# Optimization experiments

Hardware: AMD Instinct MI355X
Metric: run time of the kernel (lower is better)

Reference implementation:

```python
import jax, jax.numpy as jnp
import numpy as np

STRIDES = (4, 8, 16, 32, 64, 128)
MAPS = (128, 64, 32, 16, 8, 4)
VAR0, VAR1 = 0.1, 0.2
CLS_TH, NMS_TH, FINAL_TH = 0.05, 0.3, 0.5


def _decode_scale(ocls, oreg, stride):
    # ocls: [1,2,H,W], oreg: [1,4,H,W] -> dets [H*W, 5] = (x1,y1,x2,y2,score)
    prob = jax.nn.softmax(ocls, axis=1)[0, 1]          # [H,W] face probability
    H, W = prob.shape
    s = jnp.float32(stride)
    pcx = s / 2 + jnp.arange(W, dtype=jnp.float32)[None, :] * s   # prior center x
    pcy = s / 2 + jnp.arange(H, dtype=jnp.float32)[:, None] * s   # prior center y
    pwh = s * 4.0                                                 # prior w = h = 4*stride
    loc = oreg[0]                                                 # [4,H,W]
    cx = pcx + loc[0] * VAR0 * pwh
    cy = pcy + loc[1] * VAR0 * pwh
    w = pwh * jnp.exp(loc[2] * VAR1)
    h = pwh * jnp.exp(loc[3] * VAR1)
    x1 = cx - w / 2
    y1 = cy - h / 2
    x2 = x1 + w
    y2 = y1 + h
    return jnp.stack([x1.ravel(), y1.ravel(), x2.ravel(), y2.ravel(), prob.ravel()], axis=1)


def _nms_keep(dets, valid):
    # Greedy NMS (torch-style, +1 box convention), fixed trip count, returns keep mask.
    N = dets.shape[0]
    scores = jnp.where(valid, dets[:, 4], -jnp.inf)
    order = jnp.argsort(-scores)            # descending by score, invalid last
    b = dets[order]
    v = valid[order]
    x1, y1, x2, y2 = b[:, 0], b[:, 1], b[:, 2], b[:, 3]
    areas = (x2 - x1 + 1.0) * (y2 - y1 + 1.0)
    pos = jnp.arange(N)

    def body(i, carry):
        sup, keep = carry
        active = jnp.logical_and(jnp.logical_not(sup[i]), v[i])
        keep = keep.at[i].set(active)
        xx1 = jnp.maximum(x1[i], x1)
        yy1 = jnp.maximum(y1[i], y1)
        xx2 = jnp.minimum(x2[i], x2)
        yy2 = jnp.minimum(y2[i], y2)
        w = jnp.maximum(xx2 - xx1 + 1.0, 0.0)
        h = jnp.maximum(yy2 - yy1 + 1.0, 0.0)
        inter = w * h
        iou = inter / (areas[i] + areas - inter)
        sup = sup | (active & (iou > NMS_TH) & (pos > i))
        return sup, keep

    sup0 = jnp.logical_not(v)
    _, keep_sorted = jax.lax.fori_loop(0, N, body, (sup0, jnp.zeros(N, dtype=bool)))
    return jnp.zeros(N, dtype=bool).at[order].set(keep_sorted)


def _forward(ol1, ol2, ol3, ol4, ol5, ol6, ol7, ol8, ol9, ol10, ol11, ol12):
    olist = [ol1, ol2, ol3, ol4, ol5, ol6, ol7, ol8, ol9, ol10, ol11, ol12]
    dets = jnp.concatenate(
        [_decode_scale(olist[2 * i], olist[2 * i + 1], STRIDES[i]) for i in range(6)],
        axis=0)                              # [N,5]
    valid = dets[:, 4] > CLS_TH              # threshold stage (score > 0.05)
    # NMS selection is index logic -> constant w.r.t. differentiation
    keep = _nms_keep(jax.lax.stop_gradient(dets), valid)
    final = keep & (dets[:, 4] > FINAL_TH)   # post-NMS score > 0.5 filter
    # fixed-shape equivalent of gathering kept rows: zero out non-kept rows
    return dets * final[:, None].astype(dets.dtype)


def setup_inputs() -> dict:
    key = jax.random.key(0)
    inp = {}
    for i, hw in enumerate(MAPS):
        kc, kr, key = jax.random.split(key, 3)
        inp[f"ol{2 * i + 1}"] = jax.random.normal(kc, (1, 2, hw, hw), dtype=jnp.float32)
        inp[f"ol{2 * i + 2}"] = jax.random.normal(kr, (1, 4, hw, hw), dtype=jnp.float32)
    return inp


def reference(ol1, ol2, ol3, ol4, ol5, ol6, ol7, ol8, ol9, ol10, ol11, ol12):
    return _forward(ol1, ol2, ol3, ol4, ol5, ol6, ol7, ol8, ol9, ol10, ol11, ol12)
```

## Files before the change

### kernel.cpp

```cpp
#include <hip/hip_runtime.h>
#include <stdint.h>

#define N_TOTAL 21840
#define NA      21888
#define W_MAX   342
#define TOT_ENT 3753792u
#define NMS_TH  0.3f
#define FINAL_TH 0.5f
#define NSLICE  8
#define SCAN_T  768
#define NPUSH   11
#define GRP     4
#define NBAND   7
#define GMAX    86

struct Inputs { const float* cls[6]; const float* reg[6]; };

__device__ __forceinline__ void block_bar() {
  asm volatile("s_waitcnt lgkmcnt(0)\n\ts_barrier" ::: "memory");
}

__device__ __forceinline__ unsigned wbase_u(unsigned w) {
  return 64u * (342u * w - (w * (w - 1u)) / 2u);
}

__global__ void decode_kernel(Inputs in,
                              float* __restrict__ dx1, float* __restrict__ dy1,
                              float* __restrict__ dx2, float* __restrict__ dy2,
                              float* __restrict__ dsc,
                              unsigned long long* __restrict__ ckey,
                              unsigned int* __restrict__ Mc,
                              unsigned int* __restrict__ rank32,
                              unsigned int* __restrict__ wcnt,
                              float* __restrict__ out) {
#pragma clang fp contract(off)
  int gid = blockIdx.x * blockDim.x + threadIdx.x;
  if (gid >= N_TOTAL) return;

  rank32[gid] = 0u;
  wcnt[gid] = 0u;
  if (gid < NA - N_TOTAL) wcnt[N_TOTAL + gid] = 0u;

  int sc, local;
  if      (gid < 16384) { sc = 0; local = gid;         }
  else if (gid < 20480) { sc = 1; local = gid - 16384; }
  else if (gid < 21504) { sc = 2; local = gid - 20480; }
  else if (gid < 21760) { sc = 3; local = gid - 21504; }
  else if (gid < 21824) { sc = 4; local = gid - 21760; }
  else                  { sc = 5; local = gid - 21824; }

  const int Wd     = 128 >> sc;
  const int stride = 4 << sc;
  const int HW     = Wd * Wd;
  const int x = local & (Wd - 1);
  const int y = local >> (7 - sc);

  const float* cls = in.cls[sc];
  const float* reg = in.reg[sc];

  float c0 = cls[local];
  float c1 = cls[HW + local];
  float m  = fmaxf(c0, c1);
  float e0 = expf(c0 - m);
  float e1 = expf(c1 - m);
  float prob = e1 / (e0 + e1);

  float l0 = reg[local];
  float l1 = reg[HW + local];
  float l2 = reg[2 * HW + local];
  float l3 = reg[3 * HW + local];

  float sF  = (float)stride;
  float pcx = 0.5f * sF + (float)x * sF;
  float pcy = 0.5f * sF + (float)y * sF;
  float pwh = sF * 4.0f;

  float cx = pcx + ((l0 * 0.1f) * pwh);
  float cy = pcy + ((l1 * 0.1f) * pwh);
  float w  = pwh * expf(l2 * 0.2f);
  float h  = pwh * expf(l3 * 0.2f);
  float x1 = cx - w * 0.5f;
  float y1 = cy - h * 0.5f;
  float x2 = x1 + w;
  float y2 = y1 + h;

  dx1[gid] = x1; dy1[gid] = y1; dx2[gid] = x2; dy2[gid] = y2; dsc[gid] = prob;

  out[gid * 5 + 0] = 0.0f;
  out[gid * 5 + 1] = 0.0f;
  out[gid * 5 + 2] = 0.0f;
  out[gid * 5 + 3] = 0.0f;
  out[gid * 5 + 4] = 0.0f;

  if (prob > FINAL_TH) {
    unsigned int pos = atomicAdd(Mc, 1u);
    ckey[pos] = ((unsigned long long)__float_as_uint(prob) << 32) |
                (unsigned int)(~(unsigned int)gid);
  }
}

__global__ void __launch_bounds__(256)
rank_kernel(const unsigned long long* __restrict__ ckey,
            const unsigned int* __restrict__ Mc,
            const float* __restrict__ dx1, const float* __restrict__ dy1,
            const float* __restrict__ dx2, const float* __restrict__ dy2,
            float* __restrict__ sx1, float* __restrict__ sy1,
            float* __restrict__ sx2, float* __restrict__ sy2,
            unsigned int* __restrict__ sorig,
            unsigned int* __restrict__ rank32) {
  __shared__ unsigned long long tile[256];
  const unsigned int M = *Mc;
  if (blockIdx.x * 256u >= M) return;
  const int t = (int)threadIdx.x;
  const int p = (int)blockIdx.x * 256 + t;
  unsigned long long mykey = (p < (int)M) ? ckey[p] : 0ull;
  const int S  = (int)((M + NSLICE - 1) / NSLICE);
  const int lo = (int)blockIdx.y * S;
  const int hi = min((int)M, lo + S);
  int partial = 0;
  const int nt = (hi > lo) ? ((hi - lo + 255) >> 8) : 0;
  for (int ti = 0; ti < nt; ++ti) {
    int j = lo + ti * 256 + t;
    tile[t] = (j < hi) ? ckey[j] : 0ull;
    __syncthreads();
#pragma unroll 8
    for (int q = 0; q < 256; ++q) partial += (tile[q] > mykey) ? 1 : 0;
    __syncthreads();
  }
  if (p < (int)M) {
    unsigned int pack = (unsigned int)partial | (1u << 24);
    unsigned int old  = atomicAdd(&rank32[p], pack);
    unsigned int newv = old + pack;
    if ((newv >> 24) == NSLICE) {
      int r = (int)(newv & 0xFFFFFF);
      unsigned int orig = ~(unsigned int)(mykey & 0xffffffffull);
      sx1[r] = dx1[orig];
      sy1[r] = dy1[orig];
      sx2[r] = dx2[orig];
      sy2[r] = dy2[orig];
      sorig[r] = orig;
    }
  }
}

__global__ void __launch_bounds__(1024)
pairs_kernel(const float* __restrict__ sx1, const float* __restrict__ sy1,
             const float* __restrict__ sx2, const float* __restrict__ sy2,
             const unsigned int* __restrict__ Mc,
             unsigned long long* __restrict__ diag,
             unsigned long long* __restrict__ bandT,
             unsigned int* __restrict__ wcnt,
             unsigned short* __restrict__ rlMeta,
             unsigned long long* __restrict__ rlBits) {
#pragma clang fp contract(off)
  const int M = (int)*Mc;
  const int W = (M + 63) >> 6;
  const int rw = (int)blockIdx.y;
  const int cwg = (int)blockIdx.x << 4;
  if (rw >= W || cwg >= W || cwg + 22 < rw) return;

  const int t = (int)threadIdx.x;
  const int g = t >> 6, l = t & 63;
  const int cw = cwg + g;

  __shared__ float cx1[1024], cy1[1024], cx2[1024], cy2[1024], car[1024];
  {
    int c = (cw << 6) + l;
    if (cw < W && c < M) {
      float a = sx1[c], b = sy1[c], d = sx2[c], e = sy2[c];
      cx1[t] = a; cy1[t] = b; cx2[t] = d; cy2[t] = e;
      car[t] = (d - a + 1.0f) * (e - b + 1.0f);
    }
  }
  __syncthreads();
  if (cw >= W) return;
  const int rwg = rw >> 2, cg = cw >> 2;
  const bool isDiag = (cw == rw);
  const bool isBand = (cw < rw) && (cg >= rwg - 1);
  const bool isCsr  = (cg >= rwg + 2);
  if (!isDiag && !isBand && !isCsr) return;

  const int r = (rw << 6) + l;
  unsigned long long bits = 0ull;
  if (r < M) {
    float ax1 = sx1[r], ay1 = sy1[r], ax2 = sx2[r], ay2 = sy2[r];
    float aarea = (ax2 - ax1 + 1.0f) * (ay2 - ay1 + 1.0f);
    const int cmax = min(64, M - (cw << 6));
    const int sb = g << 6;
    for (int cc = 0; cc < cmax; ++cc) {
      float xx1 = fmaxf(ax1, cx1[sb + cc]);
      float yy1 = fmaxf(ay1, cy1[sb + cc]);
      float xx2 = fminf(ax2, cx2[sb + cc]);
      float yy2 = fminf(ay2, cy2[sb + cc]);
      float ww = fmaxf(xx2 - xx1 + 1.0f, 0.0f);
      float hh = fmaxf(yy2 - yy1 + 1.0f, 0.0f);
      float inter = ww * hh;
      float iou = inter / (aarea + car[sb + cc] - inter);
      if (iou > NMS_TH) bits |= (1ull << cc);
    }
  }
  if (isDiag)      diag[r] = bits;
  else if (isBand) bandT[(size_t)(rw - cw - 1) * NA + r] = bits;
  else {
    unsigned long long ball = __ballot(bits != 0ull);
    if (ball) {
      unsigned n_ = (unsigned)__popcll(ball);
      unsigned base = 0u;
      if (l == 0) base = atomicAdd(&wcnt[rw], n_);
      base = (unsigned)__shfl((int)base, 0);
      if (bits != 0ull) {
        unsigned rank = (unsigned)__popcll(ball & ((1ull << l) - 1ull));
        unsigned slot = wbase_u((unsigned)rw) + base + rank;
        rlMeta[slot] = (unsigned short)(((unsigned)l << 9) | (unsigned)cw);
        rlBits[slot] = bits;
      }
    }
  }
}

__global__ void __launch_bounds__(SCAN_T)
scan_kernel(const unsigned long long* __restrict__ diag,
            const unsigned long long* __restrict__ bandT,
            const unsigned int* __restrict__ wcnt,
            const unsigned short* __restrict__ rlMeta,
            const unsigned long long* __restrict__ rlBits,
            const unsigned int* __restrict__ sorig,
            const unsigned int* __restrict__ Mc,
            const float* __restrict__ dx1, const float* __restrict__ dy1,
            const float* __restrict__ dx2, const float* __restrict__ dy2,
            const float* __restrict__ dsc,
            float* __restrict__ out) {
  __shared__ unsigned long long sup[W_MAX];
  __shared__ unsigned long long kmls[W_MAX];
  __shared__ unsigned lds_wcnt[W_MAX];
  __shared__ unsigned gdone[GMAX];
  __shared__ volatile unsigned sflag;
  const int t = (int)threadIdx.x;
  const int g = t >> 6, l = t & 63;
  const int M = (int)*Mc;
  const int W = (M + 63) >> 6;
  const int NS = (W + 3) >> 2;

  for (int i = t; i < W_MAX; i += SCAN_T) {
    sup[i] = 0ull; kmls[i] = 0ull; lds_wcnt[i] = wcnt[i];
  }
  for (int i = t; i < GMAX; i += SCAN_T) gdone[i] = 0u;
  if (t == 0) sflag = 0u;
  block_bar();

  if (g == 0) {
    __builtin_amdgcn_s_setprio(1);
    const unsigned long long lowm = (1ull << l) - 1ull;
    unsigned long long dc[4], dn[4];
    unsigned long long bc[4][NBAND], bn[4][NBAND];
    unsigned long long kp[4] = {0ull, 0ull, 0ull, 0ull};
#pragma unroll
    for (int i = 0; i < 4; ++i) {
      int v = i, vc = (v < W) ? v : 0;
      dc[i] = diag[(vc << 6) + l];
#pragma unroll
      for (int d = 1; d <= NBAND; ++d)
        if (d <= i + 4) bc[i][d - 1] = bandT[(size_t)(d - 1) * NA + (vc << 6) + l];
    }
#pragma unroll
    for (int i = 0; i < 4; ++i) {
      int v = 4 + i, vc = (v < W) ? v : 0;
      dn[i] = diag[(vc << 6) + l];
#pragma unroll
      for (int d = 1; d <= NBAND; ++d)
        if (d <= i + 4) bn[i][d - 1] = bandT[(size_t)(d - 1) * NA + (vc << 6) + l];
    }
    for (int s = 0; s < NS; ++s) {
      const int v0 = s << 2;
      unsigned long long accp[4];
#pragma unroll
      for (int i = 0; i < 4; ++i) {
        unsigned long long a = 0ull;
#pragma unroll
        for (int d = 1; d <= NBAND; ++d)
          if (d <= i + 4 && d > i) a |= (bc[i][d - 1] & kp[i - d + 4]);
        accp[i] = a;
      }
      if (s >= 2) {
        while (*(volatile unsigned*)&gdone[s - 2] < (unsigned)NPUSH) {}
        asm volatile("" ::: "memory");
      }
      unsigned long long sv[4];
#pragma unroll
      for (int i = 0; i < 4; ++i)
        sv[i] = (v0 + i < W) ? sup[v0 + i] : 0ull;
      unsigned long long kc[4];
#pragma unroll
      for (int i = 0; i < 4; ++i) {
        const int v = v0 + i;
        unsigned long long kept = 0ull;
        if (v < W) {
          unsigned long long acc = accp[i];
#pragma unroll
          for (int d = 1; d <= 3; ++d)
            if (d <= i) acc |= (bc[i][d - 1] & kc[i - d]);
          unsigned long long incoming = __ballot(acc != 0ull);
          const int n = min(64, M - (v << 6));
          unsigned long long wm = (n >= 64) ? ~0ull : ((1ull << n) - 1ull);
          unsigned long long pend = (~(sv[i] | incoming)) & wm;
          const unsigned long long dv = dc[i] & lowm;
          unsigned long long dead = ~pend, und = pend;
          while (und) {
            unsigned long long bS = __ballot((dv & kept) != 0ull) & und;
            unsigned long long bK = __ballot((dv & ~dead) == 0ull) & und;
            kept |= bK; dead |= bS; und &= ~(bK | bS);
          }
          if (l == i) kmls[v] = kept;
        }
        kc[i] = kept;
      }
      asm volatile("s_waitcnt lgkmcnt(0)" ::: "memory");
      if (l == 0) sflag = (unsigned)(s + 1);
#pragma unroll
      for (int i = 0; i < 4; ++i) kp[i] = kc[i];
#pragma unroll
      for (int i = 0; i < 4; ++i) {
        dc[i] = dn[i];
#pragma unroll
        for (int d = 0; d < NBAND; ++d)
          if (d <= i + 3) bc[i][d] = bn[i][d];
      }
      const int vn = v0 + 8;
#pragma unroll
      for (int i = 0; i < 4; ++i) {
        int v = vn + i, vc = (v < W) ? v : 0;
        dn[i] = diag[(vc << 6) + l];
#pragma unroll
        for (int d = 1; d <= NBAND; ++d)
          if (d <= i + 4) bn[i][d - 1] = bandT[(size_t)(d - 1) * NA + (vc << 6) + l];
      }
    }
    __builtin_amdgcn_s_setprio(0);
  } else {
    const int p = (g - 1) * 64 + l;
    for (int s = 0; s < NS; ++s) {
      while (sflag < (unsigned)(s + 1)) __builtin_amdgcn_s_sleep(1);
      asm volatile("" ::: "memory");
      const int v0 = s << 2;
#pragma unroll
      for (int i = 0; i < 4; ++i) {
        const int v = v0 + i;
        if (v >= W) continue;
        const unsigned tw = lds_wcnt[v];
        if (tw == 0u) continue;
        const unsigned long long km = kmls[v];
        if (km == 0ull) continue;
        const unsigned base = wbase_u((unsigned)v);
        unsigned idx = base + (unsigned)p;
        const unsigned end = base + tw;
        if (idx < end) {
          unsigned mm0 = (unsigned)rlMeta[idx];
          unsigned long long bb0 = rlBits[idx];
          for (;;) {
            unsigned nidx = idx + (unsigned)(NPUSH * 64);
            bool has = (nidx < end);
            unsigned mm1 = has ? (unsigned)rlMeta[nidx] : 0u;
            unsigned long long bb1 = has ? rlBits[nidx] : 0ull;
            if ((km >> (mm0 >> 9)) & 1ull)
              atomicOr(&sup[mm0 & 511u], bb0);
            if (!has) break;
            idx = nidx; mm0 = mm1; bb0 = bb1;
          }
        }
      }
      asm volatile("s_waitcnt lgkmcnt(0)" ::: "memory");
      if (l == 0) atomicAdd(&gdone[s], 1u);
    }
  }
  block_bar();

  for (int i = t; i < (W << 6); i += SCAN_T) {
    if ((kmls[i >> 6] >> (i & 63)) & 1ull) {
      unsigned int orig = sorig[i];
      out[(size_t)orig * 5 + 0] = dx1[orig];
      out[(size_t)orig * 5 + 1] = dy1[orig];
      out[(size_t)orig * 5 + 2] = dx2[orig];
      out[(size_t)orig * 5 + 3] = dy2[orig];
      out[(size_t)orig * 5 + 4] = dsc[orig];
    }
  }
}

__global__ void __launch_bounds__(1024)
nms_kernel(const float* __restrict__ sx1, const float* __restrict__ sy1,
           const float* __restrict__ sx2, const float* __restrict__ sy2,
           const unsigned int* __restrict__ sorig,
           const unsigned int* __restrict__ Mc,
           unsigned int* __restrict__ keepflag) {
#pragma clang fp contract(off)
  __shared__ unsigned long long sup[W_MAX];
  __shared__ unsigned long long inrow[64];
  __shared__ float wx1[64], wy1[64], wx2[64], wy2[64], warea[64];
  __shared__ unsigned long long keptmask_sh;

  const int t = (int)threadIdx.x;
  const int M = (int)*Mc;
  const int W = (M + 63) >> 6;

  for (int i = t; i < W_MAX; i += 1024) sup[i] = 0ull;
  __syncthreads();

  for (int w = 0; w < W; ++w) {
    const int base = w << 6;
    const int n = min(64, M - base);
    if (t < 64) {
      if (t < n) {
        float a = sx1[base + t], b = sy1[base + t];
        float c = sx2[base + t], d = sy2[base + t];
        wx1[t] = a; wy1[t] = b; wx2[t] = c; wy2[t] = d;
        warea[t] = (c - a + 1.0f) * (d - b + 1.0f);
      }
    } else if (t < 128) {
      inrow[t - 64] = 0ull;
    }
    __syncthreads();
    {
      int r = t & 63, seg = t >> 6;
      unsigned long long bits = 0ull;
      if (r < n) {
        float ax1 = wx1[r], ay1 = wy1[r], ax2 = wx2[r], ay2 = wy2[r];
        float aarea = warea[r];
        for (int c = seg * 4; c < seg * 4 + 4; ++c) {
          if (c > r && c < n) {
            float xx1 = fmaxf(ax1, wx1[c]);
            float yy1 = fmaxf(ay1, wy1[c]);
            float xx2 = fminf(ax2, wx2[c]);
            float yy2 = fminf(ay2, wy2[c]);
            float ww = fmaxf(xx2 - xx1 + 1.0f, 0.0f);
            float hh = fmaxf(yy2 - yy1 + 1.0f, 0.0f);
            float inter = ww * hh;
            float iou = inter / (aarea + warea[c] - inter);
            if (iou > NMS_TH) bits |= (1ull << c);
          }
        }
      }
      if (bits) atomicOr(&inrow[r], bits);
    }
    __syncthreads();
    if (t < 64) {
      unsigned long long wordmask = (n >= 64) ? ~0ull : ((1ull << n) - 1ull);
      unsigned long long pending = (~sup[w]) & wordmask;
      unsigned long long kept = 0ull;
      while (pending) {
        int i = __builtin_ctzll(pending);
        kept |= (1ull << i);
        pending &= ~(inrow[i] | (1ull << i));
      }
      if (t == 0) keptmask_sh = kept;
      if (t < n && ((kept >> t) & 1ull)) keepflag[sorig[base + t]] = 1u;
    }
    __syncthreads();
    unsigned long long km = keptmask_sh;
    if (km) {
      int wid = t >> 6, lane = t & 63;
      for (int jw = w + 1 + wid; (jw << 6) < M; jw += 16) {
        int j = (jw << 6) + lane;
        bool supj = false;
        if (j < M) {
          float jx1 = sx1[j], jy1 = sy1[j], jx2 = sx2[j], jy2 = sy2[j];
          float jarea = (jx2 - jx1 + 1.0f) * (jy2 - jy1 + 1.0f);
          unsigned long long mm = km;
          while (mm) {
            int r = __builtin_ctzll(mm);
            mm &= mm - 1ull;
            float xx1 = fmaxf(wx1[r], jx1);
            float yy1 = fmaxf(wy1[r], jy1);
            float xx2 = fminf(wx2[r], jx2);
            float yy2 = fminf(wy2[r], jy2);
            float ww = fmaxf(xx2 - xx1 + 1.0f, 0.0f);
            float hh = fmaxf(yy2 - yy1 + 1.0f, 0.0f);
            float inter = ww * hh;
            float iou = inter / (warea[r] + jarea - inter);
            if (iou > NMS_TH) { supj = true; break; }
          }
        }
        unsigned long long bal = __ballot(supj);
        if (lane == 0 && bal) atomicOr(&sup[jw], bal);
      }
    }
    __syncthreads();
  }
}

__global__ void output_kernel(const float* __restrict__ dx1, const float* __restrict__ dy1,
                              const float* __restrict__ dx2, const float* __restrict__ dy2,
                              const float* __restrict__ dsc,
                              const unsigned int* __restrict__ keepflag,
                              float* __restrict__ out) {
#pragma clang fp contract(off)
  int gid = blockIdx.x * blockDim.x + threadIdx.x;
  if (gid >= N_TOTAL) return;
  float f = keepflag[gid] ? 1.0f : 0.0f;
  out[gid * 5 + 0] = dx1[gid] * f;
  out[gid * 5 + 1] = dy1[gid] * f;
  out[gid * 5 + 2] = dx2[gid] * f;
  out[gid * 5 + 3] = dy2[gid] * f;
  out[gid * 5 + 4] = dsc[gid] * f;
}

extern "C" void kernel_launch(void* const* d_in, const int* in_sizes, int n_in,
                              void* d_out, int out_size, void* d_ws, size_t ws_size,
                              hipStream_t stream) {
  (void)in_sizes; (void)n_in; (void)out_size;

  Inputs in;
  for (int i = 0; i < 6; ++i) {
    in.cls[i] = (const float*)d_in[2 * i];
    in.reg[i] = (const float*)d_in[2 * i + 1];
  }

  char* ws = (char*)d_ws;
  size_t o = 0;
  float* dx1 = (float*)(ws + o); o += (size_t)NA * 4;
  float* dy1 = (float*)(ws + o); o += (size_t)NA * 4;
  float* dx2 = (float*)(ws + o); o += (size_t)NA * 4;
  float* dy2 = (float*)(ws + o); o += (size_t)NA * 4;
  float* dsc = (float*)(ws + o); o += (size_t)NA * 4;
  unsigned long long* ckey = (unsigned long long*)(ws + o); o += (size_t)NA * 8;
  float* sx1 = (float*)(ws + o); o += (size_t)NA * 4;
  float* sy1 = (float*)(ws + o); o += (size_t)NA * 4;
  float* sx2 = (float*)(ws + o); o += (size_t)NA * 4;
  float* sy2 = (float*)(ws + o); o += (size_t)NA * 4;
  unsigned int* sorig = (unsigned int*)(ws + o); o += (size_t)NA * 4;
  unsigned int* keepflag = (unsigned int*)(ws + o); o += (size_t)NA * 4;
  unsigned int* rank32 = (unsigned int*)(ws + o); o += (size_t)NA * 4;
  unsigned int* wcnt = (unsigned int*)(ws + o); o += (size_t)NA * 4;
  unsigned int* Mc = (unsigned int*)(ws + o); o += 64;
  o = (o + 511) & ~(size_t)511;
  unsigned long long* diag = (unsigned long long*)(ws + o); o += (size_t)NA * 8;
  unsigned long long* bandT = (unsigned long long*)(ws + o); o += (size_t)NBAND * NA * 8;
  unsigned long long* rlBits = (unsigned long long*)(ws + o); o += (size_t)TOT_ENT * 8;
  unsigned short* rlMeta = (unsigned short*)(ws + o); o += (size_t)TOT_ENT * 2;
  size_t need = o;
  const bool fast = (need <= ws_size);

  const int nb = (N_TOTAL + 255) / 256;

  if (fast) {
    (void)hipMemsetAsync((void*)Mc, 0, 64, stream);
    decode_kernel<<<nb, 256, 0, stream>>>(in, dx1, dy1, dx2, dy2, dsc, ckey, Mc,
                                          rank32, wcnt, (float*)d_out);
    rank_kernel<<<dim3(nb, NSLICE), 256, 0, stream>>>(ckey, Mc, dx1, dy1, dx2, dy2,
                                                      sx1, sy1, sx2, sy2, sorig,
                                                      rank32);
    pairs_kernel<<<dim3(22, W_MAX), 1024, 0, stream>>>(sx1, sy1, sx2, sy2, Mc,
                                                       diag, bandT, wcnt, rlMeta, rlBits);
    scan_kernel<<<1, SCAN_T, 0, stream>>>(diag, bandT, wcnt, rlMeta, rlBits, sorig, Mc,
                                          dx1, dy1, dx2, dy2, dsc, (float*)d_out);
  } else {
    (void)hipMemsetAsync((void*)keepflag, 0, (size_t)NA * 12 + 64, stream);
    decode_kernel<<<nb, 256, 0, stream>>>(in, dx1, dy1, dx2, dy2, dsc, ckey, Mc,
                                          rank32, wcnt, (float*)d_out);
    rank_kernel<<<dim3(nb, NSLICE), 256, 0, stream>>>(ckey, Mc, dx1, dy1, dx2, dy2,
                                                      sx1, sy1, sx2, sy2, sorig,
                                                      rank32);
    nms_kernel<<<1, 1024, 0, stream>>>(sx1, sy1, sx2, sy2, sorig, Mc, keepflag);
    output_kernel<<<nb, 256, 0, stream>>>(dx1, dy1, dx2, dy2, dsc, keepflag,
                                          (float*)d_out);
  }
}
```

Measured before the change: 307.8 us.

## Prefetch CSR push entries two slices ahead and batch per-block atomic slot reservation

```diff
diff --git a/kernel.cpp b/kernel.cpp
--- a/kernel.cpp
+++ b/kernel.cpp
@@ -10,6 +10,7 @@
 #define NSLICE  8
 #define SCAN_T  768
 #define NPUSH   11
+#define PLANES  704
 #define GRP     4
 #define NBAND   7
 #define GMAX    86
@@ -164,6 +165,7 @@
   const int cw = cwg + g;
 
   __shared__ float cx1[1024], cy1[1024], cx2[1024], cy2[1024], car[1024];
+  __shared__ unsigned wvcnt[16], wvbase[16];
   {
     int c = (cw << 6) + l;
     if (cw < W && c < M) {
@@ -173,16 +175,17 @@
     }
   }
   __syncthreads();
-  if (cw >= W) return;
+
   const int rwg = rw >> 2, cg = cw >> 2;
-  const bool isDiag = (cw == rw);
-  const bool isBand = (cw < rw) && (cg >= rwg - 1);
-  const bool isCsr  = (cg >= rwg + 2);
-  if (!isDiag && !isBand && !isCsr) return;
+  const bool inW    = (cw < W);
+  const bool isDiag = inW && (cw == rw);
+  const bool isBand = inW && (cw < rw) && (cg >= rwg - 1);
+  const bool isCsr  = inW && (cg >= rwg + 2);
+  const bool any    = isDiag || isBand || isCsr;
 
   const int r = (rw << 6) + l;
   unsigned long long bits = 0ull;
-  if (r < M) {
+  if (any && r < M) {
     float ax1 = sx1[r], ay1 = sy1[r], ax2 = sx2[r], ay2 = sy2[r];
     float aarea = (ax2 - ax1 + 1.0f) * (ay2 - ay1 + 1.0f);
     const int cmax = min(64, M - (cw << 6));
@@ -201,20 +204,30 @@
   }
   if (isDiag)      diag[r] = bits;
   else if (isBand) bandT[(size_t)(rw - cw - 1) * NA + r] = bits;
-  else {
-    unsigned long long ball = __ballot(bits != 0ull);
-    if (ball) {
-      unsigned n_ = (unsigned)__popcll(ball);
-      unsigned base = 0u;
-      if (l == 0) base = atomicAdd(&wcnt[rw], n_);
-      base = (unsigned)__shfl((int)base, 0);
-      if (bits != 0ull) {
-        unsigned rank = (unsigned)__popcll(ball & ((1ull << l) - 1ull));
-        unsigned slot = wbase_u((unsigned)rw) + base + rank;
-        rlMeta[slot] = (unsigned short)(((unsigned)l << 9) | (unsigned)cw);
-        rlBits[slot] = bits;
-      }
-    }
+
+  unsigned long long ball = 0ull;
+  unsigned myrank = 0u;
+  {
+    bool mine = isCsr && (bits != 0ull);
+    ball = __ballot(mine);
+    myrank = (unsigned)__popcll(ball & ((1ull << l) - 1ull));
+    if (l == 0) wvcnt[g] = (unsigned)__popcll(ball);
+  }
+  __syncthreads();
+  if (t == 0) {
+    unsigned tot = 0u;
+    unsigned pre[16];
+#pragma unroll
+    for (int i = 0; i < 16; ++i) { pre[i] = tot; tot += wvcnt[i]; }
+    unsigned base = (tot != 0u) ? atomicAdd(&wcnt[rw], tot) : 0u;
+#pragma unroll
+    for (int i = 0; i < 16; ++i) wvbase[i] = base + pre[i];
+  }
+  __syncthreads();
+  if (isCsr && bits != 0ull) {
+    unsigned slot = wbase_u((unsigned)rw) + wvbase[g] + myrank;
+    rlMeta[slot] = (unsigned short)(((unsigned)l << 9) | (unsigned)cw);
+    rlBits[slot] = bits;
   }
 }
 
@@ -338,39 +351,63 @@
     __builtin_amdgcn_s_setprio(0);
   } else {
     const int p = (g - 1) * 64 + l;
+
+#define PUSH_LOAD(mX, bX, gs)                                               \
+    {                                                                       \
+      _Pragma("unroll")                                                     \
+      for (int i = 0; i < 4; ++i) {                                         \
+        int v = (gs) * 4 + i;                                               \
+        unsigned vc = (v < W) ? (unsigned)v : 0u;                           \
+        unsigned base = wbase_u(vc);                                        \
+        unsigned i0 = base + (unsigned)p;   if (i0 >= TOT_ENT) i0 = 0u;     \
+        unsigned i1 = i0 + (unsigned)PLANES; if (i1 >= TOT_ENT) i1 = 0u;    \
+        mX[i][0] = (unsigned)rlMeta[i0]; bX[i][0] = rlBits[i0];             \
+        mX[i][1] = (unsigned)rlMeta[i1]; bX[i][1] = rlBits[i1];             \
+      }                                                                     \
+    }
+
+    unsigned mA[4][2], mB[4][2];
+    unsigned long long bA[4][2], bB[4][2];
+    PUSH_LOAD(mA, bA, 0)
+    PUSH_LOAD(mB, bB, 1)
     for (int s = 0; s < NS; ++s) {
       while (sflag < (unsigned)(s + 1)) __builtin_amdgcn_s_sleep(1);
       asm volatile("" ::: "memory");
-      const int v0 = s << 2;
 #pragma unroll
       for (int i = 0; i < 4; ++i) {
-        const int v = v0 + i;
-        if (v >= W) continue;
-        const unsigned tw = lds_wcnt[v];
-        if (tw == 0u) continue;
-        const unsigned long long km = kmls[v];
-        if (km == 0ull) continue;
-        const unsigned base = wbase_u((unsigned)v);
-        unsigned idx = base + (unsigned)p;
-        const unsigned end = base + tw;
-        if (idx < end) {
-          unsigned mm0 = (unsigned)rlMeta[idx];
-          unsigned long long bb0 = rlBits[idx];
-          for (;;) {
-            unsigned nidx = idx + (unsigned)(NPUSH * 64);
-            bool has = (nidx < end);
-            unsigned mm1 = has ? (unsigned)rlMeta[nidx] : 0u;
-            unsigned long long bb1 = has ? rlBits[nidx] : 0ull;
-            if ((km >> (mm0 >> 9)) & 1ull)
-              atomicOr(&sup[mm0 & 511u], bb0);
-            if (!has) break;
-            idx = nidx; mm0 = mm1; bb0 = bb1;
+        const int v = (s << 2) + i;
+        if (v < W) {
+          const unsigned tw = lds_wcnt[v];
+          const unsigned long long km = kmls[v];
+          if (km != 0ull && tw != 0u) {
+            if ((unsigned)p < tw && ((km >> (mA[i][0] >> 9)) & 1ull))
+              atomicOr(&sup[mA[i][0] & 511u], bA[i][0]);
+            if ((unsigned)p + (unsigned)PLANES < tw &&
+                ((km >> (mA[i][1] >> 9)) & 1ull))
+              atomicOr(&sup[mA[i][1] & 511u], bA[i][1]);
+            if (tw > 2u * (unsigned)PLANES) {
+              unsigned base = wbase_u((unsigned)v);
+              for (unsigned ii = (unsigned)p + 2u * (unsigned)PLANES;
+                   ii < tw; ii += (unsigned)PLANES) {
+                unsigned sl = base + ii; if (sl >= TOT_ENT) sl = TOT_ENT - 1u;
+                unsigned mm = (unsigned)rlMeta[sl];
+                if ((km >> (mm >> 9)) & 1ull)
+                  atomicOr(&sup[mm & 511u], rlBits[sl]);
+              }
+            }
           }
         }
       }
       asm volatile("s_waitcnt lgkmcnt(0)" ::: "memory");
       if (l == 0) atomicAdd(&gdone[s], 1u);
-    }
+#pragma unroll
+      for (int i = 0; i < 4; ++i) {
+        mA[i][0] = mB[i][0]; mA[i][1] = mB[i][1];
+        bA[i][0] = bB[i][0]; bA[i][1] = bB[i][1];
+      }
+      PUSH_LOAD(mB, bB, s + 2)
+    }
+#undef PUSH_LOAD
   }
   block_bar();
 
```

After: 261.7 us. -15.0%, faster.
